# Kernel optimization log

Hardware: AMD Instinct MI355X
Metric: run time of the kernel (lower is better)

The kernel has to match this reference:

```python
import math
import jax, jax.numpy as jnp
import numpy as np

S, H, E = 8192, 4096, 64          # tokens, hidden, experts
CAPACITY_FACTOR = 1.0
MIN_CAPACITY = 4


def setup_inputs() -> dict:
    key = jax.random.key(0)
    k1, k2 = jax.random.split(key)
    return {
        "gate_input": jax.random.normal(k1, (S, H), dtype=jnp.float32),
        "gate_weight": jax.random.normal(k2, (E, H), dtype=jnp.float32) * 0.02,
    }


def reference(gate_input, gate_weight):
    # Router projection (always fp32, bias-free Linear)
    logits = gate_input.astype(jnp.float32) @ gate_weight.astype(jnp.float32).T  # [S, E]
    gates = jax.nn.softmax(logits, axis=1)
    s, e = gates.shape
    # _capacity with capacity_factor*2 for top-2; static given shapes
    capacity = max(int(math.ceil(s * (CAPACITY_FACTOR * 2.0) / e)), MIN_CAPACITY)

    # top-2 expert selection
    _, sel = jax.lax.top_k(gates, 2)                       # [S, 2]
    mask1 = jax.nn.one_hot(sel[:, 0], e, dtype=jnp.int32)  # [S, E]
    mask2 = jax.nn.one_hot(sel[:, 1], e, dtype=jnp.int32)

    # cumsum-based slot assignment within each expert
    loc1 = jnp.cumsum(mask1, axis=0) - 1
    loc2 = jnp.cumsum(mask2, axis=0) - 1 + jnp.sum(mask1, axis=0, keepdims=True)

    # aux load-balancing loss (aux_loss_coef = 0 -> no gate rescale)
    me = jnp.mean(gates, axis=0)
    ce = jnp.mean(mask1.astype(jnp.float32), axis=0)
    l_aux = jnp.mean(me * ce) * e * e

    # drop tokens over capacity
    mask1 = mask1 * (loc1 < capacity).astype(jnp.int32)
    mask2 = mask2 * (loc2 < capacity).astype(jnp.int32)
    idx_in_exp1 = jnp.sum(loc1 * mask1, axis=1)            # [S]
    idx_in_exp2 = jnp.sum(loc2 * mask2, axis=1)

    m1f = mask1.astype(jnp.float32)
    m2f = mask2.astype(jnp.float32)
    w1 = jnp.max(gates * m1f, axis=1)
    w2 = jnp.max(gates * m2f, axis=1)
    denom = jnp.maximum(w1 + w2, jnp.finfo(jnp.float32).eps)
    w1 = w1 / denom
    w2 = w2 / denom

    gates1 = w1[:, None] * m1f                             # [S, E]
    gates2 = w2[:, None] * m2f
    loc1_sc = jax.nn.one_hot(idx_in_exp1, capacity, dtype=jnp.float32)  # [S, C]
    loc2_sc = jax.nn.one_hot(idx_in_exp2, capacity, dtype=jnp.float32)
    combine_weights = (gates1[:, :, None] * loc1_sc[:, None, :]
                       + gates2[:, :, None] * loc2_sc[:, None, :])      # [S, E, C]
    dispatch_mask = combine_weights > 0
    return l_aux, combine_weights, dispatch_mask
```

## Files before the change

### kernel.cpp

```cpp
#include <hip/hip_runtime.h>
#include <cstdint>
#include <cstddef>

constexpr int S = 8192;
constexpr int H = 4096;
constexpr int E = 64;
constexpr int CAP = 256;
constexpr int KSPLIT = 8;
constexpr int KCHUNK = H / KSPLIT;
constexpr int BK = 32;
constexpr int BM = 256;
constexpr long long SEC = (long long)S * E * CAP;

__global__ __launch_bounds__(256)
void k_gemm(const float* __restrict__ A, const float* __restrict__ W,
            float* __restrict__ part, float* __restrict__ sumg,
            int* __restrict__ cnt1) {
    __shared__ float As[BK][BM + 4];
    __shared__ float Bs[BK][E + 4];
    const int tid = threadIdx.x;
    if (blockIdx.x == 0 && blockIdx.y == 0) {
        if (tid < 64) sumg[tid] = 0.f;
        else if (tid < 128) cnt1[tid - 64] = 0;
    }
    const int m0 = blockIdx.x * BM;
    const int kbase = blockIdx.y * KCHUNK;
    const int lr = tid >> 3;
    const int lc = (tid & 7) << 2;
    const int ty = tid >> 3;
    const int tx = tid & 7;

    float acc[8][8];
#pragma unroll
    for (int i = 0; i < 8; ++i)
#pragma unroll
        for (int j = 0; j < 8; ++j) acc[i][j] = 0.f;

    for (int kc = 0; kc < KCHUNK; kc += BK) {
        const float* ap = A + (size_t)(m0 + lr) * H + (kbase + kc + lc);
        float4 av[8];
#pragma unroll
        for (int j = 0; j < 8; ++j)
            av[j] = *(const float4*)(ap + (size_t)(32 * j) * H);
        const float* bp = W + (size_t)lr * H + (kbase + kc + lc);
        const float4 bv0 = *(const float4*)bp;
        const float4 bv1 = *(const float4*)(bp + (size_t)32 * H);
        __syncthreads();
#pragma unroll
        for (int j = 0; j < 8; ++j) {
            As[lc + 0][lr + 32 * j] = av[j].x;
            As[lc + 1][lr + 32 * j] = av[j].y;
            As[lc + 2][lr + 32 * j] = av[j].z;
            As[lc + 3][lr + 32 * j] = av[j].w;
        }
        Bs[lc + 0][lr] = bv0.x; Bs[lc + 1][lr] = bv0.y;
        Bs[lc + 2][lr] = bv0.z; Bs[lc + 3][lr] = bv0.w;
        Bs[lc + 0][lr + 32] = bv1.x; Bs[lc + 1][lr + 32] = bv1.y;
        Bs[lc + 2][lr + 32] = bv1.z; Bs[lc + 3][lr + 32] = bv1.w;
        __syncthreads();
#pragma unroll
        for (int kk = 0; kk < BK; ++kk) {
            const float4 a0 = *(const float4*)&As[kk][ty * 8];
            const float4 a1 = *(const float4*)&As[kk][ty * 8 + 4];
            const float4 b0 = *(const float4*)&Bs[kk][tx * 8];
            const float4 b1 = *(const float4*)&Bs[kk][tx * 8 + 4];
            const float a[8] = {a0.x, a0.y, a0.z, a0.w, a1.x, a1.y, a1.z, a1.w};
            const float b[8] = {b0.x, b0.y, b0.z, b0.w, b1.x, b1.y, b1.z, b1.w};
#pragma unroll
            for (int i = 0; i < 8; ++i)
#pragma unroll
                for (int j = 0; j < 8; ++j)
                    acc[i][j] = fmaf(a[i], b[j], acc[i][j]);
        }
    }
    float* P = part + (size_t)blockIdx.y * S * E;
#pragma unroll
    for (int i = 0; i < 8; ++i) {
        const size_t row = (size_t)(m0 + ty * 8 + i);
        float4 v0 = make_float4(acc[i][0], acc[i][1], acc[i][2], acc[i][3]);
        float4 v1 = make_float4(acc[i][4], acc[i][5], acc[i][6], acc[i][7]);
        *(float4*)&P[row * E + tx * 8] = v0;
        *(float4*)&P[row * E + tx * 8 + 4] = v1;
    }
}

__global__ __launch_bounds__(256)
void k_router(const float* __restrict__ part, int* __restrict__ e1a,
              int* __restrict__ e2a, float* __restrict__ g1a,
              float* __restrict__ g2a, float* __restrict__ sumg,
              int* __restrict__ cnt1) {
    const int lane = threadIdx.x & 63;
    const int gw = blockIdx.x * 4 + (threadIdx.x >> 6);
    float lsum = 0.f;
    int lcnt = 0;
    for (int s = gw; s < S; s += 256) {
        const float* p = part + (size_t)s * E + lane;
        float l = 0.f;
#pragma unroll
        for (int j = 0; j < KSPLIT; ++j)
            l += p[(size_t)j * S * E];
        float m = l;
#pragma unroll
        for (int o = 32; o; o >>= 1) m = fmaxf(m, __shfl_xor(m, o));
        const float ex = __expf(l - m);
        float Z = ex;
#pragma unroll
        for (int o = 32; o; o >>= 1) Z += __shfl_xor(Z, o);
        const float g = ex / Z;
        lsum += g;
        float v1 = g; int i1 = lane;
#pragma unroll
        for (int o = 32; o; o >>= 1) {
            const float ov = __shfl_xor(v1, o);
            const int oi = __shfl_xor(i1, o);
            if (ov > v1 || (ov == v1 && oi < i1)) { v1 = ov; i1 = oi; }
        }
        float v2 = (lane == i1) ? -1.f : g; int i2 = lane;
#pragma unroll
        for (int o = 32; o; o >>= 1) {
            const float ov = __shfl_xor(v2, o);
            const int oi = __shfl_xor(i2, o);
            if (ov > v2 || (ov == v2 && oi < i2)) { v2 = ov; i2 = oi; }
        }
        if (i1 == lane) lcnt++;
        if (lane == 0) {
            e1a[s] = i1; e2a[s] = i2; g1a[s] = v1; g2a[s] = v2;
        }
    }
    atomicAdd(&sumg[lane], lsum);
    atomicAdd(&cnt1[lane], lcnt);
}

__global__ __launch_bounds__(256)
void k_assign(const int* __restrict__ e1a, const int* __restrict__ e2a,
              int* __restrict__ slot1a, int* __restrict__ slot2a,
              int* __restrict__ tot1) {
    const int e = blockIdx.x;
    const int tid = threadIdx.x;
    const int lane = tid & 63;
    const int w = tid >> 6;
    __shared__ int c1[4], c2[4];
    const unsigned long long below = (1ull << lane) - 1ull;
    int cnt1 = 0, cnt2 = 0;
    int v1 = e1a[tid], v2 = e2a[tid];
    for (int c = 0; c < S; c += 256) {
        const int s = c + tid;
        const int cur1 = v1, cur2 = v2;
        if (c + 256 < S) {
            v1 = e1a[s + 256];
            v2 = e2a[s + 256];
        }
        const bool m1 = (cur1 == e);
        const bool m2 = (cur2 == e);
        const unsigned long long b1 = __ballot(m1);
        const unsigned long long b2 = __ballot(m2);
        if (lane == 0) { c1[w] = __popcll(b1); c2[w] = __popcll(b2); }
        __syncthreads();
        int pre1 = 0, pre2 = 0, t1 = 0, t2 = 0;
#pragma unroll
        for (int i = 0; i < 4; ++i) {
            const int x1 = c1[i], x2 = c2[i];
            if (i < w) { pre1 += x1; pre2 += x2; }
            t1 += x1; t2 += x2;
        }
        if (m1) {
            const int r = cnt1 + pre1 + __popcll(b1 & below);
            slot1a[s] = (r < CAP) ? r : -1;
        }
        if (m2) {
            slot2a[s] = cnt2 + pre2 + __popcll(b2 & below);
        }
        cnt1 += t1; cnt2 += t2;
        __syncthreads();
    }
    if (tid == 0) tot1[e] = cnt1;
}

__global__ __launch_bounds__(256)
void k_scatter(const int* __restrict__ e1a, const int* __restrict__ e2a,
               const float* __restrict__ g1a, const float* __restrict__ g2a,
               const int* __restrict__ slot1a, const int* __restrict__ slot2a,
               const int* __restrict__ tot1, const float* __restrict__ sumg,
               const int* __restrict__ cnt1, float* __restrict__ out) {
    const int s = blockIdx.x * 256 + threadIdx.x;
    float* comb = out + 1;
    float* mask = out + 1 + (size_t)SEC;
    const int e2 = e2a[s];
    const int sl1 = slot1a[s];
    const int r2 = slot2a[s] + tot1[e2];
    const bool ok2 = (r2 < CAP);
    const float w1 = (sl1 >= 0) ? g1a[s] : 0.f;
    const float w2 = ok2 ? g2a[s] : 0.f;
    const float denom = fmaxf(w1 + w2, 1.1920928955078125e-07f);
    if (sl1 >= 0) {
        const size_t off = ((size_t)s * E + e1a[s]) * CAP + sl1;
        comb[off] = w1 / denom;
        mask[off] = 1.f;
    }
    if (ok2) {
        const size_t off = ((size_t)s * E + e2) * CAP + r2;
        comb[off] = w2 / denom;
        mask[off] = 1.f;
    }
    if (blockIdx.x == 0 && threadIdx.x < 64) {
        const int lane = threadIdx.x;
        float v = sumg[lane] * (float)cnt1[lane];
#pragma unroll
        for (int o = 32; o; o >>= 1) v += __shfl_xor(v, o);
        if (lane == 0) out[0] = v * (float)E / ((float)S * (float)S);
    }
}

extern "C" void kernel_launch(void* const* d_in, const int* in_sizes, int n_in,
                              void* d_out, int out_size, void* d_ws,
                              size_t ws_size, hipStream_t stream) {
    const float* A = (const float*)d_in[0];
    const float* W = (const float*)d_in[1];
    float* out = (float*)d_out;

    char* ws = (char*)d_ws;
    float* part = (float*)ws;
    size_t off = (size_t)KSPLIT * S * E * sizeof(float);
    int* e1a = (int*)(ws + off);      off += (size_t)S * 4;
    int* e2a = (int*)(ws + off);      off += (size_t)S * 4;
    float* g1a = (float*)(ws + off);  off += (size_t)S * 4;
    float* g2a = (float*)(ws + off);  off += (size_t)S * 4;
    int* slot1a = (int*)(ws + off);   off += (size_t)S * 4;
    int* slot2a = (int*)(ws + off);   off += (size_t)S * 4;
    float* sumg = (float*)(ws + off); off += (size_t)E * 4;
    int* cnt1 = (int*)(ws + off);     off += (size_t)E * 4;
    int* tot1 = (int*)(ws + off);     off += (size_t)E * 4;

    hipMemsetAsync(d_out, 0, sizeof(float) * (size_t)(1 + 2 * SEC), stream);

    k_gemm<<<dim3(S / BM, KSPLIT), 256, 0, stream>>>(A, W, part, sumg, cnt1);
    k_router<<<64, 256, 0, stream>>>(part, e1a, e2a, g1a, g2a, sumg, cnt1);
    k_assign<<<E, 256, 0, stream>>>(e1a, e2a, slot1a, slot2a, tot1);
    k_scatter<<<S / 256, 256, 0, stream>>>(e1a, e2a, g1a, g2a, slot1a, slot2a,
                                           tot1, sumg, cnt1, out);
}
```

Baseline: 1.224 ms.

## Fuse output zero-fill into GEMM launch to overlap memset with router projection

Removes the separate hipMemsetAsync over the large combine/dispatch output and instead appends extra blocks to the GEMM grid that zero the output with nontemporal vector stores. The intent is for the bandwidth-bound fill to run concurrently with the compute-bound split-K GEMM instead of serially before it, and to avoid a separate launch. The risk is that fill blocks compete with GEMM blocks for CUs and memory bandwidth, and the flattened 1D grid changes the block scheduling order.

```diff
diff --git a/kernel.cpp b/kernel.cpp
--- a/kernel.cpp
+++ b/kernel.cpp
@@ -11,20 +11,40 @@
 constexpr int BK = 32;
 constexpr int BM = 256;
 constexpr long long SEC = (long long)S * E * CAP;
-
-__global__ __launch_bounds__(256)
-void k_gemm(const float* __restrict__ A, const float* __restrict__ W,
-            float* __restrict__ part, float* __restrict__ sumg,
-            int* __restrict__ cnt1) {
+constexpr int GEMM_BLOCKS = (S / BM) * KSPLIT;
+constexpr int FILL_BLOCKS = 2048;
+
+typedef float floatx4 __attribute__((ext_vector_type(4)));
+
+__global__ __launch_bounds__(256)
+void k_gemm_fill(const float* __restrict__ A, const float* __restrict__ W,
+                 float* __restrict__ part, float* __restrict__ sumg,
+                 int* __restrict__ cnt1, float* __restrict__ out) {
     __shared__ float As[BK][BM + 4];
     __shared__ float Bs[BK][E + 4];
     const int tid = threadIdx.x;
-    if (blockIdx.x == 0 && blockIdx.y == 0) {
+    const int b = blockIdx.x;
+
+    if (b >= GEMM_BLOCKS) {
+        const int fid = b - GEMM_BLOCKS;
+        const floatx4 z = {0.f, 0.f, 0.f, 0.f};
+        floatx4* o4 = (floatx4*)out;
+        const size_t n4 = (size_t)SEC / 2;
+        for (size_t i = (size_t)fid * 256 + tid; i < n4;
+             i += (size_t)FILL_BLOCKS * 256)
+            __builtin_nontemporal_store(z, &o4[i]);
+        if (fid == 0 && tid == 0) out[2 * SEC] = 0.f;
+        return;
+    }
+
+    if (b == 0) {
         if (tid < 64) sumg[tid] = 0.f;
         else if (tid < 128) cnt1[tid - 64] = 0;
     }
-    const int m0 = blockIdx.x * BM;
-    const int kbase = blockIdx.y * KCHUNK;
+    const int bx = b & 31;
+    const int by = b >> 5;
+    const int m0 = bx * BM;
+    const int kbase = by * KCHUNK;
     const int lr = tid >> 3;
     const int lc = (tid & 7) << 2;
     const int ty = tid >> 3;
@@ -65,15 +85,15 @@
             const float4 b0 = *(const float4*)&Bs[kk][tx * 8];
             const float4 b1 = *(const float4*)&Bs[kk][tx * 8 + 4];
             const float a[8] = {a0.x, a0.y, a0.z, a0.w, a1.x, a1.y, a1.z, a1.w};
-            const float b[8] = {b0.x, b0.y, b0.z, b0.w, b1.x, b1.y, b1.z, b1.w};
+            const float bb[8] = {b0.x, b0.y, b0.z, b0.w, b1.x, b1.y, b1.z, b1.w};
 #pragma unroll
             for (int i = 0; i < 8; ++i)
 #pragma unroll
                 for (int j = 0; j < 8; ++j)
-                    acc[i][j] = fmaf(a[i], b[j], acc[i][j]);
-        }
-    }
-    float* P = part + (size_t)blockIdx.y * S * E;
+                    acc[i][j] = fmaf(a[i], bb[j], acc[i][j]);
+        }
+    }
+    float* P = part + (size_t)by * S * E;
 #pragma unroll
     for (int i = 0; i < 8; ++i) {
         const size_t row = (size_t)(m0 + ty * 8 + i);
@@ -231,9 +251,8 @@
     int* cnt1 = (int*)(ws + off);     off += (size_t)E * 4;
     int* tot1 = (int*)(ws + off);     off += (size_t)E * 4;
 
-    hipMemsetAsync(d_out, 0, sizeof(float) * (size_t)(1 + 2 * SEC), stream);
-
-    k_gemm<<<dim3(S / BM, KSPLIT), 256, 0, stream>>>(A, W, part, sumg, cnt1);
+    k_gemm_fill<<<GEMM_BLOCKS + FILL_BLOCKS, 256, 0, stream>>>(
+        A, W, part, sumg, cnt1, out);
     k_router<<<64, 256, 0, stream>>>(part, e1a, e2a, g1a, g2a, sumg, cnt1);
     k_assign<<<E, 256, 0, stream>>>(e1a, e2a, slot1a, slot2a, tot1);
     k_scatter<<<S / 256, 256, 0, stream>>>(e1a, e2a, g1a, g2a, slot1a, slot2a,
```

Result: no change. 1.243 ms (+1.5%).
